# Optimization experiments

Measured on AMD Instinct MI355X. Metric: run time of the kernel, lower is better.

Reference implementation:

```python
import jax, jax.numpy as jnp
import numpy as np

N = 20000          # nodes
E = 320000         # edges (avg degree 16)
F_IN = 512         # in_channels
HID = 64           # hidden_channels
H1 = 8             # conv1 heads (hard-coded in source)
C_OUT = 7          # out_channels (num classes)
OUT2 = C_OUT * C_OUT  # conv2 per-head output dim = out_channels**2
H2 = 8             # conv2 heads
NC = 64            # number of clusters
NIDX = 10000       # |cluster_index|
NEG_SLOPE = 0.2    # PyG GATConv default leaky-relu slope


def gat_conv(x, edge_index, W, att_src, att_dst, bias, concat):
    """PyG GATConv (add_self_loops=True, eval mode so attention dropout is off)."""
    n = x.shape[0]
    H, C = att_src.shape
    h = (x @ W).reshape(n, H, C)                      # [n, H, C]
    loop = jnp.arange(n)
    src = jnp.concatenate([edge_index[0], loop])      # self loops appended
    dst = jnp.concatenate([edge_index[1], loop])
    a_src = jnp.einsum('nhc,hc->nh', h, att_src)      # [n, H]
    a_dst = jnp.einsum('nhc,hc->nh', h, att_dst)
    e = jax.nn.leaky_relu(a_src[src] + a_dst[dst], NEG_SLOPE)   # [Etot, H]
    # segment softmax over incoming edges of each destination node
    m = jax.lax.stop_gradient(jax.ops.segment_max(e, dst, num_segments=n))
    p = jnp.exp(e - m[dst])
    denom = jax.ops.segment_sum(p, dst, num_segments=n)
    alpha = p / denom[dst]                            # [Etot, H]
    out = jax.ops.segment_sum(alpha[:, :, None] * h[src], dst, num_segments=n)  # [n, H, C]
    if concat:
        return out.reshape(n, H * C) + bias
    return out.mean(axis=1) + bias


def setup_inputs() -> dict:
    key = jax.random.key(0)
    ks = jax.random.split(key, 12)
    s1 = 1.0 / np.sqrt(F_IN)
    s2 = 1.0 / np.sqrt(2 * HID * H1)
    return {
        'x': jax.random.normal(ks[0], (N, F_IN), dtype=jnp.float32),
        'edge_index': jax.random.randint(ks[1], (2, E), 0, N),
        'cluster_id': jax.random.uniform(ks[2], (N, NC), dtype=jnp.float32),
        'cluster_index': jax.random.randint(ks[3], (NIDX,), 0, N),
        'W1': jax.random.normal(ks[4], (F_IN, H1 * HID), dtype=jnp.float32) * s1,
        'att_src1': jax.random.normal(ks[5], (H1, HID), dtype=jnp.float32) * 0.1,
        'att_dst1': jax.random.normal(ks[6], (H1, HID), dtype=jnp.float32) * 0.1,
        'b1': jnp.zeros((H1 * HID,), dtype=jnp.float32),
        'W2': jax.random.normal(ks[7], (2 * H1 * HID, H2 * OUT2), dtype=jnp.float32) * s2,
        'att_src2': jax.random.normal(ks[8], (H2, OUT2), dtype=jnp.float32) * 0.1,
        'att_dst2': jax.random.normal(ks[9], (H2, OUT2), dtype=jnp.float32) * 0.1,
        'b2': jnp.zeros((OUT2,), dtype=jnp.float32),
    }


def reference(x, edge_index, cluster_id, cluster_index,
              W1, att_src1, att_dst1, b1, W2, att_src2, att_dst2, b2):
    n = x.shape[0]
    # eval mode: F.dropout and attention dropout are identity
    h = jax.nn.elu(gat_conv(x, edge_index, W1, att_src1, att_dst1, b1, concat=True))  # [N, H1*HID]
    cid = cluster_id[cluster_index]                       # [NIDX, NC]
    cluster_features = (cid.T @ h[cluster_index]) / cid.sum(0)[:, None]  # [NC, H1*HID]
    x1 = cluster_features[jnp.argmax(cluster_id, axis=1)] # [N, H1*HID]
    xx = jnp.concatenate([jnp.concatenate([h, x1], 1),
                          jnp.concatenate([x1, h], 1)], 0)  # [2N, 2*H1*HID]
    ei2 = jnp.concatenate([edge_index, edge_index + n], 1)  # doubled graph
    return gat_conv(xx, ei2, W2, att_src2, att_dst2, b2, concat=False)  # [2N, OUT2]
```

## Files before the change

### kernel.cpp

```cpp
#include <hip/hip_runtime.h>

#define NNODES 20000
#define MPAD   20096
#define NEDGES 320000
#define FIN    512
#define HC1    512
#define NHEAD  8
#define OUT2   49
#define NCOL2  392
#define NB2    784
#define NPAD2  896
#define NCLU   64
#define NIDX   10000
#define NEG    0.2f

typedef unsigned short u16;
typedef short bf16x8 __attribute__((ext_vector_type(8)));
typedef float f32x4 __attribute__((ext_vector_type(4)));

static __device__ __forceinline__ float lrelu(float v){ return v > 0.f ? v : NEG*v; }

static __device__ __forceinline__ u16 f2bf_hi(float f, float& rem) {
  union { float f; unsigned u; } c; c.f = f;
  unsigned hb = c.u & 0xFFFF0000u;
  union { unsigned u; float f; } d; d.u = hb;
  rem = f - d.f;
  return (u16)(hb >> 16);
}
static __device__ __forceinline__ u16 f2bf(float f) {
  union { float f; unsigned u; } c; c.f = f;
  return (u16)(c.u >> 16);
}
static __device__ __forceinline__ u16 f2bf_rn(float f) {
  union { float f; unsigned u; } c; c.f = f;
  unsigned r = c.u + 0x7FFFu + ((c.u >> 16) & 1u);
  return (u16)(r >> 16);
}
static __device__ __forceinline__ float bf2f(u16 u) {
  union { unsigned u; float f; } c; c.u = ((unsigned)u) << 16;
  return c.f;
}
static __device__ __forceinline__ void load8bf(const u16* p, float* o) {
  ushort4 a = *(const ushort4*)p;
  ushort4 b = *(const ushort4*)(p + 4);
  o[0]=bf2f(a.x); o[1]=bf2f(a.y); o[2]=bf2f(a.z); o[3]=bf2f(a.w);
  o[4]=bf2f(b.x); o[5]=bf2f(b.y); o[6]=bf2f(b.z); o[7]=bf2f(b.w);
}

typedef __attribute__((address_space(3))) unsigned int lds_u32;
typedef __attribute__((address_space(1))) const unsigned int glb_u32;
static __device__ __forceinline__ void gl_lds16(const u16* g, u16* l) {
  __builtin_amdgcn_global_load_lds((glb_u32*)g, (lds_u32*)l, 16, 0, 0);
}

__global__ __launch_bounds__(256) void split4_kernel(const float* __restrict__ x,
                                                     u16* __restrict__ xh, u16* __restrict__ xl) {
  __shared__ __align__(16) u16 th[4][512], tl[4][512];
  int wv = threadIdx.x >> 6;
  int lane = threadIdx.x & 63;
  int i = blockIdx.x*4 + wv;
  const float* p = x + (size_t)i*FIN + lane*8;
  float4 v0 = *(const float4*)p, v1 = *(const float4*)(p+4);
  float rem; ushort4 h0,h1,l0,l1;
  h0.x = f2bf_hi(v0.x, rem); l0.x = f2bf(rem);
  h0.y = f2bf_hi(v0.y, rem); l0.y = f2bf(rem);
  h0.z = f2bf_hi(v0.z, rem); l0.z = f2bf(rem);
  h0.w = f2bf_hi(v0.w, rem); l0.w = f2bf(rem);
  h1.x = f2bf_hi(v1.x, rem); l1.x = f2bf(rem);
  h1.y = f2bf_hi(v1.y, rem); l1.y = f2bf(rem);
  h1.z = f2bf_hi(v1.z, rem); l1.z = f2bf(rem);
  h1.w = f2bf_hi(v1.w, rem); l1.w = f2bf(rem);
  *(ushort4*)&th[wv][lane*8]   = h0; *(ushort4*)&th[wv][lane*8+4] = h1;
  *(ushort4*)&tl[wv][lane*8]   = l0; *(ushort4*)&tl[wv][lane*8+4] = l1;
  __syncthreads();
  int kc = threadIdx.x >> 2, nd = threadIdx.x & 3;
  size_t o = ((size_t)kc*MPAD + blockIdx.x*4 + nd)*8;
  *(uint4*)&xh[o] = *(const uint4*)&th[nd][kc*8];
  *(uint4*)&xl[o] = *(const uint4*)&tl[nd][kc*8];
}

__global__ void tw1_kernel(const float* __restrict__ W1, u16* __restrict__ Th, u16* __restrict__ Tl) {
  int tid = blockIdx.x*256 + threadIdx.x;
  int kc = tid >> 9, j = tid & 511;
  float rem; ushort4 h0,h1,l0,l1;
  h0.x = f2bf_hi(W1[(size_t)(kc*8+0)*512 + j], rem); l0.x = f2bf(rem);
  h0.y = f2bf_hi(W1[(size_t)(kc*8+1)*512 + j], rem); l0.y = f2bf(rem);
  h0.z = f2bf_hi(W1[(size_t)(kc*8+2)*512 + j], rem); l0.z = f2bf(rem);
  h0.w = f2bf_hi(W1[(size_t)(kc*8+3)*512 + j], rem); l0.w = f2bf(rem);
  h1.x = f2bf_hi(W1[(size_t)(kc*8+4)*512 + j], rem); l1.x = f2bf(rem);
  h1.y = f2bf_hi(W1[(size_t)(kc*8+5)*512 + j], rem); l1.y = f2bf(rem);
  h1.z = f2bf_hi(W1[(size_t)(kc*8+6)*512 + j], rem); l1.z = f2bf(rem);
  h1.w = f2bf_hi(W1[(size_t)(kc*8+7)*512 + j], rem); l1.w = f2bf(rem);
  size_t o = ((size_t)kc*512 + j)*8;
  *(ushort4*)&Th[o] = h0; *(ushort4*)&Th[o+4] = h1;
  *(ushort4*)&Tl[o] = l0; *(ushort4*)&Tl[o+4] = l1;
}

__global__ void tb2_kernel(const float* __restrict__ W2, u16* __restrict__ Th, u16* __restrict__ Tl) {
  int tid = blockIdx.x*256 + threadIdx.x;
  int kc = tid / NPAD2, j = tid - kc*NPAD2;
  float v[8];
  #pragma unroll
  for (int e = 0; e < 8; e++) {
    int k = kc*8 + e;
    v[e] = (j < NCOL2) ? W2[(size_t)k*NCOL2 + j]
         : ((j < NB2) ? W2[(size_t)(512+k)*NCOL2 + (j - NCOL2)] : 0.f);
  }
  float rem; ushort4 h0,h1,l0,l1;
  h0.x = f2bf_hi(v[0], rem); l0.x = f2bf(rem);
  h0.y = f2bf_hi(v[1], rem); l0.y = f2bf(rem);
  h0.z = f2bf_hi(v[2], rem); l0.z = f2bf(rem);
  h0.w = f2bf_hi(v[3], rem); l0.w = f2bf(rem);
  h1.x = f2bf_hi(v[4], rem); l1.x = f2bf(rem);
  h1.y = f2bf_hi(v[5], rem); l1.y = f2bf(rem);
  h1.z = f2bf_hi(v[6], rem); l1.z = f2bf(rem);
  h1.w = f2bf_hi(v[7], rem); l1.w = f2bf(rem);
  size_t o = ((size_t)kc*NPAD2 + j)*8;
  *(ushort4*)&Th[o] = h0; *(ushort4*)&Th[o+4] = h1;
  *(ushort4*)&Tl[o] = l0; *(ushort4*)&Tl[o+4] = l1;
}

template<int EPI>
__global__ __launch_bounds__(256) void gemm_mfma(
    const u16* __restrict__ Ah, const u16* __restrict__ Al,
    const u16* __restrict__ Bh, const u16* __restrict__ Bl,
    int Apitch, int Bpitch,
    u16* __restrict__ Cbf, int M, int Ncols,
    const int* __restrict__ cmax, const float* __restrict__ CFW, u16* __restrict__ h2)
{
  __shared__ __align__(16) u16 S[16512];
  int tid = threadIdx.x;
  int lane = tid & 63;
  int w = tid >> 6;
  int row0 = blockIdx.x * 128;
  int col0 = blockIdx.y * 128;

  const u16* G; size_t pitch; int lb;
  if      (w == 0) { G = Ah + ((size_t)row0 + lane)*8; pitch = (size_t)Apitch; lb = 0; }
  else if (w == 1) { G = Al + ((size_t)row0 + lane)*8; pitch = (size_t)Apitch; lb = 4128; }
  else if (w == 2) { G = Bh + ((size_t)col0 + lane)*8; pitch = (size_t)Bpitch; lb = 8256; }
  else             { G = Bl + ((size_t)col0 + lane)*8; pitch = (size_t)Bpitch; lb = 12384; }

  int wr = (w >> 1) * 64;
  int wc = (w & 1) * 64;
  int l16 = lane & 15;
  int q = lane >> 4;

  f32x4 acc[4][4];
  #pragma unroll
  for (int i = 0; i < 4; i++)
    #pragma unroll
    for (int j = 0; j < 4; j++)
      acc[i][j] = (f32x4){0.f, 0.f, 0.f, 0.f};

  for (int t = 0; t < 16; t++) {
    #pragma unroll
    for (int c = 0; c < 4; c++) {
      const u16* g = G + ((size_t)(t*4 + c))*pitch*8;
      gl_lds16(g,       &S[lb + c*1032]);
      gl_lds16(g + 512, &S[lb + c*1032 + 512]);
    }
    __syncthreads();
    bf16x8 ah[4], al[4], bh[4], bl[4];
    #pragma unroll
    for (int i = 0; i < 4; i++) {
      int ra = q*1032 + (wr + i*16 + l16)*8;
      int rb = q*1032 + (wc + i*16 + l16)*8;
      ah[i] = *(const bf16x8*)&S[ra];
      al[i] = *(const bf16x8*)&S[4128 + ra];
      bh[i] = *(const bf16x8*)&S[8256 + rb];
      bl[i] = *(const bf16x8*)&S[12384 + rb];
    }
    #pragma unroll
    for (int i = 0; i < 4; i++)
      #pragma unroll
      for (int j = 0; j < 4; j++)
        acc[i][j] = __builtin_amdgcn_mfma_f32_16x16x32_bf16(ah[i], bh[j], acc[i][j], 0, 0, 0);
    #pragma unroll
    for (int i = 0; i < 4; i++)
      #pragma unroll
      for (int j = 0; j < 4; j++)
        acc[i][j] = __builtin_amdgcn_mfma_f32_16x16x32_bf16(ah[i], bl[j], acc[i][j], 0, 0, 0);
    #pragma unroll
    for (int i = 0; i < 4; i++)
      #pragma unroll
      for (int j = 0; j < 4; j++)
        acc[i][j] = __builtin_amdgcn_mfma_f32_16x16x32_bf16(al[i], bh[j], acc[i][j], 0, 0, 0);
    __syncthreads();
  }

  if (EPI == 0) {
    #pragma unroll
    for (int i = 0; i < 4; i++) {
      #pragma unroll
      for (int r = 0; r < 4; r++) {
        int m = row0 + wr + i*16 + q*4 + r;
        if (m < M) {
          #pragma unroll
          for (int j = 0; j < 4; j++)
            Cbf[(size_t)m*Ncols + col0 + wc + j*16 + l16] = f2bf_rn(acc[i][j][r]);
        }
      }
    }
  } else {
    #pragma unroll
    for (int i = 0; i < 4; i++) {
      #pragma unroll
      for (int r = 0; r < 4; r++) {
        int m = row0 + wr + i*16 + q*4 + r;
        if (m >= M) continue;
        int c = cmax[m];
        const float* cf = CFW + (size_t)c * NB2;
        #pragma unroll
        for (int j = 0; j < 4; j++) {
          int n = col0 + wc + j*16 + l16;
          if (n >= NB2) continue;
          float v = acc[i][j][r];
          if (n < NCOL2) h2[(size_t)m*NCOL2 + n] = f2bf_rn(v + cf[NCOL2 + n]);
          else           h2[(size_t)(NNODES + m)*NCOL2 + (n - NCOL2)] = f2bf_rn(v + cf[n - NCOL2]);
        }
      }
    }
  }
}

__global__ void hist_kernel(const int* __restrict__ ei, int* __restrict__ counts) {
  int e = blockIdx.x*256 + threadIdx.x;
  if (e < NEDGES) atomicAdd(&counts[ei[NEDGES + e]], 1);
}

__global__ __launch_bounds__(1024) void scan_kernel(const int* __restrict__ counts,
                                                    int* __restrict__ rowptr, int* __restrict__ cursor) {
  __shared__ int part[1024];
  int t = threadIdx.x;
  const int CH = 20;
  int start = t*CH;
  int end = min(start+CH, NNODES);
  int sum = 0;
  for (int i = start; i < end; i++) sum += counts[i];
  part[t] = sum;
  __syncthreads();
  for (int off = 1; off < 1024; off <<= 1) {
    int v = part[t];
    int add = (t >= off) ? part[t-off] : 0;
    __syncthreads();
    part[t] = v + add;
    __syncthreads();
  }
  int run = part[t] - sum;
  for (int i = start; i < end; i++) {
    rowptr[i] = run; cursor[i] = run;
    run += counts[i];
  }
  if (t == 1023) rowptr[NNODES] = part[1023];
}

__global__ void scatter_kernel(const int* __restrict__ ei, int* __restrict__ cursor, int* __restrict__ csr) {
  int e = blockIdx.x*256 + threadIdx.x;
  if (e < NEDGES) {
    int src = ei[e];
    int dst = ei[NEDGES + e];
    int pos = atomicAdd(&cursor[dst], 1);
    csr[pos] = src;
  }
}

__global__ __launch_bounds__(256) void a1_kernel(
    const u16* __restrict__ hpre, const float* __restrict__ atts, const float* __restrict__ attd,
    float* __restrict__ as1, float* __restrict__ ad1)
{
  int lane = threadIdx.x & 63;
  int i = blockIdx.x*4 + (threadIdx.x >> 6);
  float hv[8];
  load8bf(hpre + (size_t)i*HC1 + lane*8, hv);
  const float* ap = atts + lane*8; const float* dp = attd + lane*8;
  float ps = 0.f, pd = 0.f;
  #pragma unroll
  for (int k = 0; k < 8; k++) { ps = fmaf(hv[k], ap[k], ps); pd = fmaf(hv[k], dp[k], pd); }
  ps += __shfl_down(ps, 4, 8); ps += __shfl_down(ps, 2, 8); ps += __shfl_down(ps, 1, 8);
  pd += __shfl_down(pd, 4, 8); pd += __shfl_down(pd, 2, 8); pd += __shfl_down(pd, 1, 8);
  if ((lane & 7) == 0) {
    as1[i*8 + (lane >> 3)] = ps;
    ad1[i*8 + (lane >> 3)] = pd;
  }
}

__global__ __launch_bounds__(256) void softmax1_kernel(
    const float* __restrict__ as1, const float* __restrict__ ad1,
    const int* __restrict__ rp, const int* __restrict__ csr,
    float* __restrict__ p1, float* __restrict__ selfw, float* __restrict__ invs)
{
  int gid = blockIdx.x*256 + threadIdx.x;
  int i = gid >> 3, h = gid & 7;
  int rs = rp[i], re = rp[i+1];
  float adst = ad1[gid];
  float ps = __expf(lrelu(as1[gid] + adst));
  float s = ps;
  for (int j = rs; j < re; j++) {
    float p = __expf(lrelu(as1[csr[j]*8 + h] + adst));
    p1[(size_t)j*8 + h] = p;
    s += p;
  }
  float inv = 1.f / s;
  selfw[gid] = ps * inv;
  invs[gid] = inv;
}

__global__ __launch_bounds__(256) void softmax2_kernel(
    const float* __restrict__ as2, const float* __restrict__ ad2,
    const int* __restrict__ rp, const int* __restrict__ csr,
    float* __restrict__ p2, float* __restrict__ selfw, float* __restrict__ invs)
{
  int gid = blockIdx.x*256 + threadIdx.x;
  int u = gid >> 3, h = gid & 7;
  int bn = (u < NNODES) ? u : u - NNODES;
  int off = u - bn;
  size_t eoff = (u < NNODES) ? 0 : NEDGES;
  int rs = rp[bn], re = rp[bn+1];
  float adst = ad2[gid];
  float ps = __expf(lrelu(as2[gid] + adst));
  float s = ps;
  for (int j = rs; j < re; j++) {
    float p = __expf(lrelu(as2[(csr[j]+off)*8 + h] + adst));
    p2[(eoff + (size_t)j)*8 + h] = p;
    s += p;
  }
  float inv = 1.f / s;
  selfw[gid] = ps * inv;
  invs[gid] = inv;
}

__global__ __launch_bounds__(256) void agg1_kernel(
    const u16* __restrict__ hpre, const float* __restrict__ p1,
    const float* __restrict__ selfw, const float* __restrict__ invs,
    const int* __restrict__ rowptr, const int* __restrict__ csr, const float* __restrict__ b1,
    u16* __restrict__ hhr, u16* __restrict__ hlr,
    u16* __restrict__ hh, u16* __restrict__ hl)
{
  __shared__ __align__(16) u16 sh[4][512], sl[4][512];
  int lane = threadIdx.x & 63;
  int wv = threadIdx.x >> 6;
  int i = blockIdx.x*4 + wv;
  int hd = lane >> 3;
  int rs = rowptr[i];
  int deg = rowptr[i+1] - rs;
  float inv = invs[i*8 + hd];
  float asf = selfw[i*8 + hd];
  float acc[8];
  {
    float v[8];
    load8bf(hpre + (size_t)i*HC1 + lane*8, v);
    #pragma unroll
    for (int k = 0; k < 8; k++) acc[k] = asf * v[k];
  }
  int j = 0;
  for (; j + 1 < deg; j += 2) {
    int s0 = csr[rs+j], s1 = csr[rs+j+1];
    float al0 = p1[(size_t)(rs+j)*8 + hd] * inv;
    float al1 = p1[(size_t)(rs+j+1)*8 + hd] * inv;
    float v0[8], v1[8];
    load8bf(hpre + (size_t)s0*HC1 + lane*8, v0);
    load8bf(hpre + (size_t)s1*HC1 + lane*8, v1);
    #pragma unroll
    for (int k = 0; k < 8; k++) acc[k] = fmaf(al0, v0[k], acc[k]);
    #pragma unroll
    for (int k = 0; k < 8; k++) acc[k] = fmaf(al1, v1[k], acc[k]);
  }
  if (j < deg) {
    int s0 = csr[rs+j];
    float al0 = p1[(size_t)(rs+j)*8 + hd] * inv;
    float v0[8];
    load8bf(hpre + (size_t)s0*HC1 + lane*8, v0);
    #pragma unroll
    for (int k = 0; k < 8; k++) acc[k] = fmaf(al0, v0[k], acc[k]);
  }
  float rem; ushort4 h0,h1,l0,l1;
  float o[8];
  #pragma unroll
  for (int k = 0; k < 8; k++) {
    float v = acc[k] + b1[lane*8 + k];
    o[k] = v > 0.f ? v : __expf(v) - 1.f;
  }
  h0.x = f2bf_hi(o[0], rem); l0.x = f2bf(rem);
  h0.y = f2bf_hi(o[1], rem); l0.y = f2bf(rem);
  h0.z = f2bf_hi(o[2], rem); l0.z = f2bf(rem);
  h0.w = f2bf_hi(o[3], rem); l0.w = f2bf(rem);
  h1.x = f2bf_hi(o[4], rem); l1.x = f2bf(rem);
  h1.y = f2bf_hi(o[5], rem); l1.y = f2bf(rem);
  h1.z = f2bf_hi(o[6], rem); l1.z = f2bf(rem);
  h1.w = f2bf_hi(o[7], rem); l1.w = f2bf(rem);
  size_t rb = (size_t)i*HC1 + lane*8;
  *(ushort4*)&hhr[rb]   = h0; *(ushort4*)&hhr[rb+4] = h1;
  *(ushort4*)&hlr[rb]   = l0; *(ushort4*)&hlr[rb+4] = l1;
  *(ushort4*)&sh[wv][lane*8]   = h0; *(ushort4*)&sh[wv][lane*8+4] = h1;
  *(ushort4*)&sl[wv][lane*8]   = l0; *(ushort4*)&sl[wv][lane*8+4] = l1;
  __syncthreads();
  int kc = threadIdx.x >> 2, nd = threadIdx.x & 3;
  size_t po = ((size_t)kc*MPAD + blockIdx.x*4 + nd)*8;
  *(uint4*)&hh[po] = *(const uint4*)&sh[nd][kc*8];
  *(uint4*)&hl[po] = *(const uint4*)&sl[nd][kc*8];
}

__global__ __launch_bounds__(256) void colsum_kernel(
    const float* __restrict__ cluster_id, const int* __restrict__ cidx, float* __restrict__ colsum)
{
  __shared__ float part[4][64];
  int tid = threadIdx.x; int q = tid >> 6, col = tid & 63;
  int start = blockIdx.x*313, end = min(start+313, NIDX);
  float acc = 0.f;
  for (int t = start + q; t < end; t += 4) {
    int node = cidx[t];
    acc += cluster_id[(size_t)node*NCLU + col];
  }
  part[q][col] = acc;
  __syncthreads();
  if (tid < 64) {
    float v = part[0][tid] + part[1][tid] + part[2][tid] + part[3][tid];
    atomicAdd(&colsum[tid], v);
  }
}

__global__ __launch_bounds__(256) void cf_kernel(
    const float* __restrict__ cluster_id, const int* __restrict__ cidx,
    const u16* __restrict__ hhr, const u16* __restrict__ hlr, float* __restrict__ CFraw)
{
  int chl = threadIdx.x & 63;
  int cq  = threadIdx.x >> 6;
  int chg = blockIdx.x*64 + chl;
  int start = blockIdx.y*400, end = start + 400;
  float acc[16];
  #pragma unroll
  for (int k = 0; k < 16; k++) acc[k] = 0.f;
  #pragma unroll 2
  for (int t = start; t < end; t++) {
    int node = cidx[t];
    size_t hi = (size_t)node*HC1 + chg;
    float hv = bf2f(hhr[hi]) + bf2f(hlr[hi]);
    const float* cp = cluster_id + (size_t)node*NCLU + cq*16;
    float4 c0 = *(const float4*)cp,     c1 = *(const float4*)(cp+4);
    float4 c2 = *(const float4*)(cp+8), c3 = *(const float4*)(cp+12);
    acc[0]  = fmaf(c0.x, hv, acc[0]);  acc[1]  = fmaf(c0.y, hv, acc[1]);
    acc[2]  = fmaf(c0.z, hv, acc[2]);  acc[3]  = fmaf(c0.w, hv, acc[3]);
    acc[4]  = fmaf(c1.x, hv, acc[4]);  acc[5]  = fmaf(c1.y, hv, acc[5]);
    acc[6]  = fmaf(c1.z, hv, acc[6]);  acc[7]  = fmaf(c1.w, hv, acc[7]);
    acc[8]  = fmaf(c2.x, hv, acc[8]);  acc[9]  = fmaf(c2.y, hv, acc[9]);
    acc[10] = fmaf(c2.z, hv, acc[10]); acc[11] = fmaf(c2.w, hv, acc[11]);
    acc[12] = fmaf(c3.x, hv, acc[12]); acc[13] = fmaf(c3.y, hv, acc[13]);
    acc[14] = fmaf(c3.z, hv, acc[14]); acc[15] = fmaf(c3.w, hv, acc[15]);
  }
  #pragma unroll
  for (int k = 0; k < 16; k++)
    atomicAdd(&CFraw[(size_t)(cq*16 + k)*HC1 + chg], acc[k]);
}

__global__ __launch_bounds__(256) void argmax_kernel(const float* __restrict__ cluster_id, int* __restrict__ cmax)
{
  int lane = threadIdx.x & 63;
  int i = blockIdx.x*4 + (threadIdx.x >> 6);
  float v = cluster_id[(size_t)i*NCLU + lane];
  int idx = lane;
  #pragma unroll
  for (int off = 32; off > 0; off >>= 1) {
    float ov = __shfl_xor(v, off);
    int oi = __shfl_xor(idx, off);
    if (ov > v || (ov == v && oi < idx)) { v = ov; idx = oi; }
  }
  if (lane == 0) cmax[i] = idx;
}

__global__ __launch_bounds__(256) void cfw_kernel(
    const float* __restrict__ CFraw, const float* __restrict__ colsum,
    const float* __restrict__ W2, float* __restrict__ CFW)
{
  int o = blockIdx.x*256 + threadIdx.x;
  int c = o / NB2, j = o - c*NB2;
  const float* src = (j < NCOL2) ? (W2 + j) : (W2 + (size_t)512*NCOL2 + (j - NCOL2));
  float acc = 0.f;
  for (int k = 0; k < 512; k++) acc = fmaf(CFraw[(size_t)c*512 + k], src[(size_t)k*NCOL2], acc);
  CFW[o] = acc / colsum[c];
}

__global__ __launch_bounds__(256) void a2_kernel(
    const u16* __restrict__ h2, const float* __restrict__ atts, const float* __restrict__ attd,
    float* __restrict__ as2, float* __restrict__ ad2)
{
  __shared__ float rows[32*NCOL2];
  __shared__ float sa[NCOL2], sd[NCOL2];
  int tid = threadIdx.x;
  size_t base = (size_t)blockIdx.x * 32 * NCOL2;
  for (int idx = tid; idx < 32*NCOL2; idx += 256) rows[idx] = bf2f(h2[base + idx]);
  for (int idx = tid; idx < NCOL2; idx += 256) { sa[idx] = atts[idx]; sd[idx] = attd[idx]; }
  __syncthreads();
  int r = tid >> 3, hd = tid & 7;
  const float* rp = rows + r*NCOL2 + hd*OUT2;
  const float* ap = sa + hd*OUT2;
  const float* dp = sd + hd*OUT2;
  float ps = 0.f, pd = 0.f;
  #pragma unroll
  for (int j = 0; j < OUT2; j++) { float v = rp[j]; ps = fmaf(v, ap[j], ps); pd = fmaf(v, dp[j], pd); }
  int node = blockIdx.x*32 + r;
  as2[node*8 + hd] = ps;
  ad2[node*8 + hd] = pd;
}

__global__ __launch_bounds__(256) void agg2_kernel(
    const u16* __restrict__ h2, const float* __restrict__ p2,
    const float* __restrict__ selfw, const float* __restrict__ invs,
    const int* __restrict__ rowptr, const int* __restrict__ csr, const float* __restrict__ b2,
    float* __restrict__ out)
{
  __shared__ float red[4][NCOL2];
  int lane = threadIdx.x & 63;
  int w = threadIdx.x >> 6;
  int u = blockIdx.x*4 + w;
  int bn = (u < NNODES) ? u : u - NNODES;
  int off = u - bn;
  int rs = rowptr[bn];
  int deg = rowptr[bn+1] - rs;
  size_t pbase = (size_t)rs + (off ? NEDGES : 0);
  int hk[7]; float invk[7];
  #pragma unroll
  for (int k = 0; k < 7; k++) {
    int c = lane + 64*k;
    int hx = (c < NCOL2) ? (c / OUT2) : 0;
    hk[k] = hx;
    invk[k] = (c < NCOL2) ? invs[u*8 + hx] : 0.f;
  }
  float acc[7];
  {
    const u16* own = h2 + (size_t)u*NCOL2;
    #pragma unroll
    for (int k = 0; k < 7; k++) {
      int c = lane + 64*k;
      acc[k] = (c < NCOL2) ? selfw[u*8 + hk[k]] * bf2f(own[c]) : 0.f;
    }
  }
  int j = 0;
  for (; j + 1 < deg; j += 2) {
    int s0 = csr[rs+j] + off, s1 = csr[rs+j+1] + off;
    const float* pp0 = p2 + (pbase + j)*8;
    const float* pp1 = pp0 + 8;
    const u16* r0 = h2 + (size_t)s0*NCOL2;
    const u16* r1 = h2 + (size_t)s1*NCOL2;
    #pragma unroll
    for (int k = 0; k < 6; k++) {
      int c = lane + 64*k;
      acc[k] = fmaf(pp0[hk[k]]*invk[k], bf2f(r0[c]), acc[k]);
      acc[k] = fmaf(pp1[hk[k]]*invk[k], bf2f(r1[c]), acc[k]);
    }
    if (lane < 8) {
      int c = lane + 384;
      acc[6] = fmaf(pp0[hk[6]]*invk[6], bf2f(r0[c]), acc[6]);
      acc[6] = fmaf(pp1[hk[6]]*invk[6], bf2f(r1[c]), acc[6]);
    }
  }
  if (j < deg) {
    int s0 = csr[rs+j] + off;
    const float* pp0 = p2 + (pbase + j)*8;
    const u16* r0 = h2 + (size_t)s0*NCOL2;
    #pragma unroll
    for (int k = 0; k < 6; k++) {
      int c = lane + 64*k;
      acc[k] = fmaf(pp0[hk[k]]*invk[k], bf2f(r0[c]), acc[k]);
    }
    if (lane < 8) acc[6] = fmaf(pp0[hk[6]]*invk[6], bf2f(r0[lane+384]), acc[6]);
  }
  #pragma unroll
  for (int k = 0; k < 7; k++) { int c = lane + 64*k; if (c < NCOL2) red[w][c] = acc[k]; }
  __syncthreads();
  if (lane < OUT2) {
    float t = 0.f;
    #pragma unroll
    for (int h = 0; h < 8; h++) t += red[w][h*OUT2 + lane];
    out[(size_t)u*OUT2 + lane] = 0.125f*t + b2[lane];
  }
}

extern "C" void kernel_launch(void* const* d_in, const int* in_sizes, int n_in,
                              void* d_out, int out_size, void* d_ws, size_t ws_size,
                              hipStream_t stream)
{
  (void)in_sizes; (void)n_in; (void)out_size; (void)ws_size;
  const float* x     = (const float*)d_in[0];
  const int*   ei    = (const int*)d_in[1];
  const float* cid   = (const float*)d_in[2];
  const int*   cidx  = (const int*)d_in[3];
  const float* W1    = (const float*)d_in[4];
  const float* atts1 = (const float*)d_in[5];
  const float* attd1 = (const float*)d_in[6];
  const float* b1    = (const float*)d_in[7];
  const float* W2    = (const float*)d_in[8];
  const float* atts2 = (const float*)d_in[9];
  const float* attd2 = (const float*)d_in[10];
  const float* b2    = (const float*)d_in[11];
  float* out = (float*)d_out;

  char* ws = (char*)d_ws;
  size_t off = 0;
  auto alloc = [&](size_t b){ size_t r = off; off += (b + 255) & ~(size_t)255; return r; };
  size_t o_hpre = alloc((size_t)NNODES*HC1*2);
  size_t o_h2   = alloc((size_t)2*NNODES*NCOL2*2);
  size_t o_xh   = alloc((size_t)64*MPAD*8*2);
  size_t o_xl   = alloc((size_t)64*MPAD*8*2);
  size_t o_hh   = alloc((size_t)64*MPAD*8*2);
  size_t o_hl   = alloc((size_t)64*MPAD*8*2);
  size_t o_hhr  = alloc((size_t)NNODES*HC1*2);
  size_t o_hlr  = alloc((size_t)NNODES*HC1*2);
  size_t o_w1h  = alloc((size_t)64*512*8*2);
  size_t o_w1l  = alloc((size_t)64*512*8*2);
  size_t o_b2h  = alloc((size_t)64*NPAD2*8*2);
  size_t o_b2l  = alloc((size_t)64*NPAD2*8*2);
  size_t o_CFW  = alloc((size_t)NCLU*NB2*4);
  size_t o_as1  = alloc((size_t)NNODES*8*4);
  size_t o_ad1  = alloc((size_t)NNODES*8*4);
  size_t o_as2  = alloc((size_t)2*NNODES*8*4);
  size_t o_ad2  = alloc((size_t)2*NNODES*8*4);
  size_t o_p1   = alloc((size_t)NEDGES*8*4);
  size_t o_p2   = alloc((size_t)2*NEDGES*8*4);
  size_t o_sw1  = alloc((size_t)NNODES*8*4);
  size_t o_iv1  = alloc((size_t)NNODES*8*4);
  size_t o_sw2  = alloc((size_t)2*NNODES*8*4);
  size_t o_iv2  = alloc((size_t)2*NNODES*8*4);
  size_t o_rp   = alloc((size_t)(NNODES+1)*4);
  size_t o_cur  = alloc((size_t)NNODES*4);
  size_t o_csr  = alloc((size_t)NEDGES*4);
  size_t o_cmax = alloc((size_t)NNODES*4);
  size_t o_cnt  = alloc((size_t)NNODES*4);
  size_t o_csum = alloc(256 + (size_t)NCLU*HC1*4);

  u16*   hpre  = (u16*)(ws + o_hpre);
  u16*   h2    = (u16*)(ws + o_h2);
  u16*   xh    = (u16*)(ws + o_xh);
  u16*   xl    = (u16*)(ws + o_xl);
  u16*   hh    = (u16*)(ws + o_hh);
  u16*   hl    = (u16*)(ws + o_hl);
  u16*   hhr   = (u16*)(ws + o_hhr);
  u16*   hlr   = (u16*)(ws + o_hlr);
  u16*   w1h   = (u16*)(ws + o_w1h);
  u16*   w1l   = (u16*)(ws + o_w1l);
  u16*   b2h   = (u16*)(ws + o_b2h);
  u16*   b2l   = (u16*)(ws + o_b2l);
  float* CFW   = (float*)(ws + o_CFW);
  float* as1   = (float*)(ws + o_as1);
  float* ad1   = (float*)(ws + o_ad1);
  float* as2   = (float*)(ws + o_as2);
  float* ad2   = (float*)(ws + o_ad2);
  float* p1    = (float*)(ws + o_p1);
  float* p2    = (float*)(ws + o_p2);
  float* sw1   = (float*)(ws + o_sw1);
  float* iv1   = (float*)(ws + o_iv1);
  float* sw2   = (float*)(ws + o_sw2);
  float* iv2   = (float*)(ws + o_iv2);
  int*   rp    = (int*)(ws + o_rp);
  int*   cur   = (int*)(ws + o_cur);
  int*   csr   = (int*)(ws + o_csr);
  int*   cmax  = (int*)(ws + o_cmax);
  int*   cnt   = (int*)(ws + o_cnt);
  float* colsum= (float*)(ws + o_csum);
  float* CFraw = (float*)(ws + o_csum + 256);

  hipMemsetAsync(ws + o_cnt, 0, (size_t)NNODES*4, stream);
  hipMemsetAsync(ws + o_csum, 0, 256 + (size_t)NCLU*HC1*4, stream);

  split4_kernel<<<5000, 256, 0, stream>>>(x, xh, xl);
  tw1_kernel<<<128, 256, 0, stream>>>(W1, w1h, w1l);
  tb2_kernel<<<224, 256, 0, stream>>>(W2, b2h, b2l);
  hist_kernel<<<1250, 256, 0, stream>>>(ei, cnt);
  scan_kernel<<<1, 1024, 0, stream>>>(cnt, rp, cur);
  scatter_kernel<<<1250, 256, 0, stream>>>(ei, cur, csr);
  gemm_mfma<0><<<dim3(157,4), 256, 0, stream>>>(xh, xl, w1h, w1l, MPAD, 512, hpre, NNODES, 512, nullptr, nullptr, nullptr);
  a1_kernel<<<5000, 256, 0, stream>>>(hpre, atts1, attd1, as1, ad1);
  softmax1_kernel<<<625, 256, 0, stream>>>(as1, ad1, rp, csr, p1, sw1, iv1);
  agg1_kernel<<<5000, 256, 0, stream>>>(hpre, p1, sw1, iv1, rp, csr, b1, hhr, hlr, hh, hl);
  colsum_kernel<<<32, 256, 0, stream>>>(cid, cidx, colsum);
  cf_kernel<<<dim3(8,25), 256, 0, stream>>>(cid, cidx, hhr, hlr, CFraw);
  argmax_kernel<<<5000, 256, 0, stream>>>(cid, cmax);
  cfw_kernel<<<196, 256, 0, stream>>>(CFraw, colsum, W2, CFW);
  gemm_mfma<1><<<dim3(157,7), 256, 0, stream>>>(hh, hl, b2h, b2l, MPAD, NPAD2, nullptr, NNODES, NB2, cmax, CFW, h2);
  a2_kernel<<<1250, 256, 0, stream>>>(h2, atts2, attd2, as2, ad2);
  softmax2_kernel<<<1250, 256, 0, stream>>>(as2, ad2, rp, csr, p2, sw2, iv2);
  agg2_kernel<<<10000, 256, 0, stream>>>(h2, p2, sw2, iv2, rp, csr, b2, out);
}
```

Baseline: 736.9 us.

## Replace per-node softmax kernels with edge-parallel exp and deferred normalization

The per-(node,head) serial softmax loops are replaced by edge-parallel kernels that compute unnormalized exp weights for all 8 heads with vectorized loads, using a new destination-id array written during CSR scatter. The softmax denominator is now accumulated inside the aggregation kernels, which normalize once at the end, so the separate selfw/invs buffers are no longer needed. agg2 is also remapped so each 8-lane group handles one head with a 4-edge unroll. This removes load imbalance and long serial dependency chains in the softmax phase. In exchange it adds an extra CSR-sized index array and leaves numerics unstabilized by max-subtraction, as before.

```diff
diff --git a/kernel.cpp b/kernel.cpp
--- a/kernel.cpp
+++ b/kernel.cpp
@@ -255,13 +255,15 @@
   if (t == 1023) rowptr[NNODES] = part[1023];
 }
 
-__global__ void scatter_kernel(const int* __restrict__ ei, int* __restrict__ cursor, int* __restrict__ csr) {
+__global__ void scatter_kernel(const int* __restrict__ ei, int* __restrict__ cursor,
+                               int* __restrict__ csr, int* __restrict__ dstid) {
   int e = blockIdx.x*256 + threadIdx.x;
   if (e < NEDGES) {
     int src = ei[e];
     int dst = ei[NEDGES + e];
     int pos = atomicAdd(&cursor[dst], 1);
     csr[pos] = src;
+    dstid[pos] = dst;
   }
 }
 
@@ -285,54 +287,50 @@
   }
 }
 
-__global__ __launch_bounds__(256) void softmax1_kernel(
-    const float* __restrict__ as1, const float* __restrict__ ad1,
-    const int* __restrict__ rp, const int* __restrict__ csr,
-    float* __restrict__ p1, float* __restrict__ selfw, float* __restrict__ invs)
-{
-  int gid = blockIdx.x*256 + threadIdx.x;
-  int i = gid >> 3, h = gid & 7;
-  int rs = rp[i], re = rp[i+1];
-  float adst = ad1[gid];
-  float ps = __expf(lrelu(as1[gid] + adst));
-  float s = ps;
-  for (int j = rs; j < re; j++) {
-    float p = __expf(lrelu(as1[csr[j]*8 + h] + adst));
-    p1[(size_t)j*8 + h] = p;
-    s += p;
-  }
-  float inv = 1.f / s;
-  selfw[gid] = ps * inv;
-  invs[gid] = inv;
-}
-
-__global__ __launch_bounds__(256) void softmax2_kernel(
-    const float* __restrict__ as2, const float* __restrict__ ad2,
-    const int* __restrict__ rp, const int* __restrict__ csr,
-    float* __restrict__ p2, float* __restrict__ selfw, float* __restrict__ invs)
-{
-  int gid = blockIdx.x*256 + threadIdx.x;
-  int u = gid >> 3, h = gid & 7;
-  int bn = (u < NNODES) ? u : u - NNODES;
-  int off = u - bn;
-  size_t eoff = (u < NNODES) ? 0 : NEDGES;
-  int rs = rp[bn], re = rp[bn+1];
-  float adst = ad2[gid];
-  float ps = __expf(lrelu(as2[gid] + adst));
-  float s = ps;
-  for (int j = rs; j < re; j++) {
-    float p = __expf(lrelu(as2[(csr[j]+off)*8 + h] + adst));
-    p2[(eoff + (size_t)j)*8 + h] = p;
-    s += p;
-  }
-  float inv = 1.f / s;
-  selfw[gid] = ps * inv;
-  invs[gid] = inv;
+__global__ void exp1_kernel(const int* __restrict__ csr, const int* __restrict__ dstid,
+                            const float* __restrict__ as1, const float* __restrict__ ad1,
+                            float* __restrict__ p1)
+{
+  int pos = blockIdx.x*256 + threadIdx.x;
+  int src = csr[pos], dst = dstid[pos];
+  const float* a = as1 + (size_t)src*8;
+  const float* d = ad1 + (size_t)dst*8;
+  float4 a0 = *(const float4*)a, a1v = *(const float4*)(a+4);
+  float4 d0 = *(const float4*)d, d1v = *(const float4*)(d+4);
+  float4 o0, o1;
+  o0.x = __expf(lrelu(a0.x + d0.x));  o0.y = __expf(lrelu(a0.y + d0.y));
+  o0.z = __expf(lrelu(a0.z + d0.z));  o0.w = __expf(lrelu(a0.w + d0.w));
+  o1.x = __expf(lrelu(a1v.x + d1v.x)); o1.y = __expf(lrelu(a1v.y + d1v.y));
+  o1.z = __expf(lrelu(a1v.z + d1v.z)); o1.w = __expf(lrelu(a1v.w + d1v.w));
+  *(float4*)(p1 + (size_t)pos*8)     = o0;
+  *(float4*)(p1 + (size_t)pos*8 + 4) = o1;
+}
+
+__global__ void exp2_kernel(const int* __restrict__ csr, const int* __restrict__ dstid,
+                            const float* __restrict__ as2, const float* __restrict__ ad2,
+                            float* __restrict__ p2)
+{
+  int pos2 = blockIdx.x*256 + threadIdx.x;
+  int half = (pos2 >= NEDGES) ? 1 : 0;
+  int pos = pos2 - half*NEDGES;
+  int src = csr[pos] + half*NNODES;
+  int dst = dstid[pos] + half*NNODES;
+  const float* a = as2 + (size_t)src*8;
+  const float* d = ad2 + (size_t)dst*8;
+  float4 a0 = *(const float4*)a, a1v = *(const float4*)(a+4);
+  float4 d0 = *(const float4*)d, d1v = *(const float4*)(d+4);
+  float4 o0, o1;
+  o0.x = __expf(lrelu(a0.x + d0.x));  o0.y = __expf(lrelu(a0.y + d0.y));
+  o0.z = __expf(lrelu(a0.z + d0.z));  o0.w = __expf(lrelu(a0.w + d0.w));
+  o1.x = __expf(lrelu(a1v.x + d1v.x)); o1.y = __expf(lrelu(a1v.y + d1v.y));
+  o1.z = __expf(lrelu(a1v.z + d1v.z)); o1.w = __expf(lrelu(a1v.w + d1v.w));
+  *(float4*)(p2 + (size_t)pos2*8)     = o0;
+  *(float4*)(p2 + (size_t)pos2*8 + 4) = o1;
 }
 
 __global__ __launch_bounds__(256) void agg1_kernel(
     const u16* __restrict__ hpre, const float* __restrict__ p1,
-    const float* __restrict__ selfw, const float* __restrict__ invs,
+    const float* __restrict__ as1, const float* __restrict__ ad1,
     const int* __restrict__ rowptr, const int* __restrict__ csr, const float* __restrict__ b1,
     u16* __restrict__ hhr, u16* __restrict__ hlr,
     u16* __restrict__ hh, u16* __restrict__ hl)
@@ -344,41 +342,44 @@
   int hd = lane >> 3;
   int rs = rowptr[i];
   int deg = rowptr[i+1] - rs;
-  float inv = invs[i*8 + hd];
-  float asf = selfw[i*8 + hd];
+  float selfp = __expf(lrelu(as1[i*8 + hd] + ad1[i*8 + hd]));
   float acc[8];
   {
     float v[8];
     load8bf(hpre + (size_t)i*HC1 + lane*8, v);
     #pragma unroll
-    for (int k = 0; k < 8; k++) acc[k] = asf * v[k];
-  }
+    for (int k = 0; k < 8; k++) acc[k] = selfp * v[k];
+  }
+  float s = selfp;
   int j = 0;
   for (; j + 1 < deg; j += 2) {
     int s0 = csr[rs+j], s1 = csr[rs+j+1];
-    float al0 = p1[(size_t)(rs+j)*8 + hd] * inv;
-    float al1 = p1[(size_t)(rs+j+1)*8 + hd] * inv;
+    float w0 = p1[(size_t)(rs+j)*8 + hd];
+    float w1 = p1[(size_t)(rs+j+1)*8 + hd];
     float v0[8], v1[8];
     load8bf(hpre + (size_t)s0*HC1 + lane*8, v0);
     load8bf(hpre + (size_t)s1*HC1 + lane*8, v1);
     #pragma unroll
-    for (int k = 0; k < 8; k++) acc[k] = fmaf(al0, v0[k], acc[k]);
-    #pragma unroll
-    for (int k = 0; k < 8; k++) acc[k] = fmaf(al1, v1[k], acc[k]);
+    for (int k = 0; k < 8; k++) acc[k] = fmaf(w0, v0[k], acc[k]);
+    #pragma unroll
+    for (int k = 0; k < 8; k++) acc[k] = fmaf(w1, v1[k], acc[k]);
+    s += w0 + w1;
   }
   if (j < deg) {
     int s0 = csr[rs+j];
-    float al0 = p1[(size_t)(rs+j)*8 + hd] * inv;
+    float w0 = p1[(size_t)(rs+j)*8 + hd];
     float v0[8];
     load8bf(hpre + (size_t)s0*HC1 + lane*8, v0);
     #pragma unroll
-    for (int k = 0; k < 8; k++) acc[k] = fmaf(al0, v0[k], acc[k]);
-  }
+    for (int k = 0; k < 8; k++) acc[k] = fmaf(w0, v0[k], acc[k]);
+    s += w0;
+  }
+  float inv = 1.f / s;
   float rem; ushort4 h0,h1,l0,l1;
   float o[8];
   #pragma unroll
   for (int k = 0; k < 8; k++) {
-    float v = acc[k] + b1[lane*8 + k];
+    float v = acc[k]*inv + b1[lane*8 + k];
     o[k] = v > 0.f ? v : __expf(v) - 1.f;
   }
   h0.x = f2bf_hi(o[0], rem); l0.x = f2bf(rem);
@@ -505,7 +506,7 @@
 
 __global__ __launch_bounds__(256) void agg2_kernel(
     const u16* __restrict__ h2, const float* __restrict__ p2,
-    const float* __restrict__ selfw, const float* __restrict__ invs,
+    const float* __restrict__ as2, const float* __restrict__ ad2,
     const int* __restrict__ rowptr, const int* __restrict__ csr, const float* __restrict__ b2,
     float* __restrict__ out)
 {
@@ -518,55 +519,51 @@
   int rs = rowptr[bn];
   int deg = rowptr[bn+1] - rs;
   size_t pbase = (size_t)rs + (off ? NEDGES : 0);
-  int hk[7]; float invk[7];
-  #pragma unroll
-  for (int k = 0; k < 7; k++) {
-    int c = lane + 64*k;
-    int hx = (c < NCOL2) ? (c / OUT2) : 0;
-    hk[k] = hx;
-    invk[k] = (c < NCOL2) ? invs[u*8 + hx] : 0.f;
-  }
+  int hd = lane >> 3, sub = lane & 7;
+  int cbase = hd*OUT2 + sub;
+  float selfp = __expf(lrelu(as2[u*8 + hd] + ad2[u*8 + hd]));
   float acc[7];
   {
-    const u16* own = h2 + (size_t)u*NCOL2;
+    const u16* own = h2 + (size_t)u*NCOL2 + cbase;
+    #pragma unroll
+    for (int k = 0; k < 7; k++)
+      acc[k] = (sub + 8*k < OUT2) ? selfp * bf2f(own[8*k]) : 0.f;
+  }
+  float s = selfp;
+  int j = 0;
+  for (; j + 3 < deg; j += 4) {
+    int s0 = csr[rs+j]   + off, s1 = csr[rs+j+1] + off;
+    int s2 = csr[rs+j+2] + off, s3 = csr[rs+j+3] + off;
+    float w0 = p2[(pbase+j)*8   + hd], w1 = p2[(pbase+j+1)*8 + hd];
+    float w2 = p2[(pbase+j+2)*8 + hd], w3 = p2[(pbase+j+3)*8 + hd];
+    const u16* r0 = h2 + (size_t)s0*NCOL2 + cbase;
+    const u16* r1 = h2 + (size_t)s1*NCOL2 + cbase;
+    const u16* r2 = h2 + (size_t)s2*NCOL2 + cbase;
+    const u16* r3 = h2 + (size_t)s3*NCOL2 + cbase;
     #pragma unroll
     for (int k = 0; k < 7; k++) {
-      int c = lane + 64*k;
-      acc[k] = (c < NCOL2) ? selfw[u*8 + hk[k]] * bf2f(own[c]) : 0.f;
+      if (sub + 8*k < OUT2) {
+        acc[k] = fmaf(w0, bf2f(r0[8*k]), acc[k]);
+        acc[k] = fmaf(w1, bf2f(r1[8*k]), acc[k]);
+        acc[k] = fmaf(w2, bf2f(r2[8*k]), acc[k]);
+        acc[k] = fmaf(w3, bf2f(r3[8*k]), acc[k]);
+      }
     }
-  }
-  int j = 0;
-  for (; j + 1 < deg; j += 2) {
-    int s0 = csr[rs+j] + off, s1 = csr[rs+j+1] + off;
-    const float* pp0 = p2 + (pbase + j)*8;
-    const float* pp1 = pp0 + 8;
-    const u16* r0 = h2 + (size_t)s0*NCOL2;
-    const u16* r1 = h2 + (size_t)s1*NCOL2;
-    #pragma unroll
-    for (int k = 0; k < 6; k++) {
-      int c = lane + 64*k;
-      acc[k] = fmaf(pp0[hk[k]]*invk[k], bf2f(r0[c]), acc[k]);
-      acc[k] = fmaf(pp1[hk[k]]*invk[k], bf2f(r1[c]), acc[k]);
-    }
-    if (lane < 8) {
-      int c = lane + 384;
-      acc[6] = fmaf(pp0[hk[6]]*invk[6], bf2f(r0[c]), acc[6]);
-      acc[6] = fmaf(pp1[hk[6]]*invk[6], bf2f(r1[c]), acc[6]);
-    }
-  }
-  if (j < deg) {
+    s += (w0 + w1) + (w2 + w3);
+  }
+  for (; j < deg; j++) {
     int s0 = csr[rs+j] + off;
-    const float* pp0 = p2 + (pbase + j)*8;
-    const u16* r0 = h2 + (size_t)s0*NCOL2;
-    #pragma unroll
-    for (int k = 0; k < 6; k++) {
-      int c = lane + 64*k;
-      acc[k] = fmaf(pp0[hk[k]]*invk[k], bf2f(r0[c]), acc[k]);
-    }
-    if (lane < 8) acc[6] = fmaf(pp0[hk[6]]*invk[6], bf2f(r0[lane+384]), acc[6]);
-  }
-  #pragma unroll
-  for (int k = 0; k < 7; k++) { int c = lane + 64*k; if (c < NCOL2) red[w][c] = acc[k]; }
+    float w0 = p2[(pbase+j)*8 + hd];
+    const u16* r0 = h2 + (size_t)s0*NCOL2 + cbase;
+    #pragma unroll
+    for (int k = 0; k < 7; k++)
+      if (sub + 8*k < OUT2) acc[k] = fmaf(w0, bf2f(r0[8*k]), acc[k]);
+    s += w0;
+  }
+  float inv = 1.f / s;
+  #pragma unroll
+  for (int k = 0; k < 7; k++)
+    if (sub + 8*k < OUT2) red[w][cbase + 8*k] = acc[k] * inv;
   __syncthreads();
   if (lane < OUT2) {
     float t = 0.f;
@@ -617,13 +614,10 @@
   size_t o_ad2  = alloc((size_t)2*NNODES*8*4);
   size_t o_p1   = alloc((size_t)NEDGES*8*4);
   size_t o_p2   = alloc((size_t)2*NEDGES*8*4);
-  size_t o_sw1  = alloc((size_t)NNODES*8*4);
-  size_t o_iv1  = alloc((size_t)NNODES*8*4);
-  size_t o_sw2  = alloc((size_t)2*NNODES*8*4);
-  size_t o_iv2  = alloc((size_t)2*NNODES*8*4);
   size_t o_rp   = alloc((size_t)(NNODES+1)*4);
   size_t o_cur  = alloc((size_t)NNODES*4);
   size_t o_csr  = alloc((size_t)NEDGES*4);
+  size_t o_dst  = alloc((size_t)NEDGES*4);
   size_t o_cmax = alloc((size_t)NNODES*4);
   size_t o_cnt  = alloc((size_t)NNODES*4);
   size_t o_csum = alloc(256 + (size_t)NCLU*HC1*4);
@@ -647,13 +641,10 @@
   float* ad2   = (float*)(ws + o_ad2);
   float* p1    = (float*)(ws + o_p1);
   float* p2    = (float*)(ws + o_p2);
-  float* sw1   = (float*)(ws + o_sw1);
-  float* iv1   = (float*)(ws + o_iv1);
-  float* sw2   = (float*)(ws + o_sw2);
-  float* iv2   = (float*)(ws + o_iv2);
   int*   rp    = (int*)(ws + o_rp);
   int*   cur   = (int*)(ws + o_cur);
   int*   csr   = (int*)(ws + o_csr);
+  int*   dstid = (int*)(ws + o_dst);
   int*   cmax  = (int*)(ws + o_cmax);
   int*   cnt   = (int*)(ws + o_cnt);
   float* colsum= (float*)(ws + o_csum);
@@ -667,17 +658,17 @@
   tb2_kernel<<<224, 256, 0, stream>>>(W2, b2h, b2l);
   hist_kernel<<<1250, 256, 0, stream>>>(ei, cnt);
   scan_kernel<<<1, 1024, 0, stream>>>(cnt, rp, cur);
-  scatter_kernel<<<1250, 256, 0, stream>>>(ei, cur, csr);
+  scatter_kernel<<<1250, 256, 0, stream>>>(ei, cur, csr, dstid);
   gemm_mfma<0><<<dim3(157,4), 256, 0, stream>>>(xh, xl, w1h, w1l, MPAD, 512, hpre, NNODES, 512, nullptr, nullptr, nullptr);
   a1_kernel<<<5000, 256, 0, stream>>>(hpre, atts1, attd1, as1, ad1);
-  softmax1_kernel<<<625, 256, 0, stream>>>(as1, ad1, rp, csr, p1, sw1, iv1);
-  agg1_kernel<<<5000, 256, 0, stream>>>(hpre, p1, sw1, iv1, rp, csr, b1, hhr, hlr, hh, hl);
+  exp1_kernel<<<1250, 256, 0, stream>>>(csr, dstid, as1, ad1, p1);
+  agg1_kernel<<<5000, 256, 0, stream>>>(hpre, p1, as1, ad1, rp, csr, b1, hhr, hlr, hh, hl);
   colsum_kernel<<<32, 256, 0, stream>>>(cid, cidx, colsum);
   cf_kernel<<<dim3(8,25), 256, 0, stream>>>(cid, cidx, hhr, hlr, CFraw);
   argmax_kernel<<<5000, 256, 0, stream>>>(cid, cmax);
   cfw_kernel<<<196, 256, 0, stream>>>(CFraw, colsum, W2, CFW);
   gemm_mfma<1><<<dim3(157,7), 256, 0, stream>>>(hh, hl, b2h, b2l, MPAD, NPAD2, nullptr, NNODES, NB2, cmax, CFW, h2);
   a2_kernel<<<1250, 256, 0, stream>>>(h2, atts2, attd2, as2, ad2);
-  softmax2_kernel<<<1250, 256, 0, stream>>>(as2, ad2, rp, csr, p2, sw2, iv2);
-  agg2_kernel<<<10000, 256, 0, stream>>>(h2, p2, sw2, iv2, rp, csr, b2, out);
-}
+  exp2_kernel<<<2500, 256, 0, stream>>>(csr, dstid, as2, ad2, p2);
+  agg2_kernel<<<10000, 256, 0, stream>>>(h2, p2, as2, ad2, rp, csr, b2, out);
+}
```

Result: faster. 689.9 us (-6.4%).
